# Optimization experiments

Measured on AMD Instinct MI355X. Metric: run time of the kernel, lower is better.

Reference implementation:

```python
import jax, jax.numpy as jnp
import numpy as np

H = 256       # hidden_size
W2V = 300     # word embedding dim
POS = 30      # pos embedding dim
NF = 100      # filters per n-gram CNN
VOCAB = 50000
NPOS = 100
N_EDUS = 1024
L = 20        # tokens per EDU


def setup_inputs() -> dict:
    key = jax.random.key(0)
    ks = jax.random.split(key, 22)
    def nrm(k, shape, s=0.05):
        return jax.random.normal(k, shape, dtype=jnp.float32) * s
    cw = W2V + POS  # CNN input width = 330
    # valid transition sequence: S, then (S, R) repeated n-1 times -> 2n-1 steps
    transes = jnp.concatenate([jnp.zeros((1,), jnp.int32),
                               jnp.tile(jnp.array([0, 1], jnp.int32), N_EDUS - 1)])
    return {
        "edu_words": jax.random.randint(ks[0], (N_EDUS, L), 0, VOCAB),
        "edu_poses": jax.random.randint(ks[1], (N_EDUS, L), 0, NPOS),
        "transes": transes,
        "word_emb": nrm(ks[2], (VOCAB, W2V), 1.0),
        "pos_emb": nrm(ks[3], (NPOS, POS), 1.0),
        "Wu": nrm(ks[4], (NF, 1, 1, cw)), "bu": nrm(ks[5], (NF,)),
        "Wb": nrm(ks[6], (NF, 1, 2, cw)), "bb": nrm(ks[7], (NF,)),
        "Wt": nrm(ks[8], (NF, 1, 3, cw)), "bt": nrm(ks[9], (NF,)),
        "Wp": nrm(ks[10], (2 * H, 2 * W2V + POS + 3 * NF)), "bp": nrm(ks[11], (2 * H,)),
        "Wih": nrm(ks[12], (4 * H, 3 * H)), "Whh": nrm(ks[13], (4 * H, H)),
        "bih": nrm(ks[14], (4 * H,)), "bhh": nrm(ks[15], (4 * H,)),
        "Wc": nrm(ks[16], (5 * H, 3 * H)), "bc": nrm(ks[17], (5 * H,)),
        "Ws": nrm(ks[18], (2, H)), "bs": nrm(ks[19], (2,)),
    }


def _encode_edus(edu_words, edu_poses, word_emb, pos_emb, Wu, bu, Wb, bb, Wt, bt, Wp, bp):
    we = word_emb[edu_words]                # [N, L, 300]
    pe = pos_emb[edu_poses]                 # [N, L, 30]
    x = jnp.concatenate([we, pe], axis=-1)[:, None, :, :]  # NCHW [N,1,L,330]
    def conv_pool(W, b, pad):
        # kernel spans full width -> output width 1; pad only along time
        y = jax.lax.conv_general_dilated(x, W, (1, 1), ((pad, pad), (0, 0)),
                                         dimension_numbers=("NCHW", "OIHW", "NCHW"))[..., 0]
        return jax.nn.relu(y + b[None, :, None]).max(axis=-1)  # [N, F]
    feats = jnp.concatenate([we[:, 0], we[:, -1], pe[:, 0],
                             conv_pool(Wu, bu, 0), conv_pool(Wb, bb, 1),
                             conv_pool(Wt, bt, 2)], axis=-1)   # [N, 930]
    h, c = jnp.split(feats @ Wp.T + bp, 2, axis=-1)
    return h, c


def _parse_loss(edu_words, edu_poses, transes, word_emb, pos_emb, Wu, bu, Wb, bb, Wt, bt,
                Wp, bp, Wih, Whh, bih, bhh, Wc, bc, Ws, bs):
    eh, ec = _encode_edus(edu_words, edu_poses, word_emb, pos_emb, Wu, bu, Wb, bb, Wt, bt, Wp, bp)
    M = N_EDUS + 2
    buf_h = jnp.concatenate([eh, jnp.zeros((2, H), jnp.float32)], axis=0)
    buf_c = jnp.concatenate([ec, jnp.zeros((2, H), jnp.float32)], axis=0)
    stack_h = jnp.zeros((M, H), jnp.float32)  # slots 0,1 are the initial placeholders
    stack_c = jnp.zeros((M, H), jnp.float32)

    def lstm(xv, h, c):  # torch LSTMCell gate order i,f,g,o
        g = xv @ Wih.T + bih + h @ Whh.T + bhh
        i, f, gg, o = jnp.split(g, 4)
        c2 = jax.nn.sigmoid(f) * c + jax.nn.sigmoid(i) * jnp.tanh(gg)
        return jax.nn.sigmoid(o) * jnp.tanh(c2), c2

    def track(sh, sptr, bptr, th, tc):
        xv = jnp.concatenate([sh[sptr - 1], sh[sptr - 2], buf_h[bptr]])
        return lstm(xv, th, tc)

    sptr = jnp.int32(2)
    bptr = jnp.int32(0)
    th, tc = track(stack_h, sptr, bptr, jnp.zeros(H, jnp.float32), jnp.zeros(H, jnp.float32))

    def step(carry, trans):
        sh, sc, sptr, bptr, th, tc = carry
        logits = th @ Ws.T + bs  # scorer MLP with mlp_layers=1 -> single Linear
        is_shift = trans == 0
        # SHIFT candidate: push buffer front
        sh_s = sh.at[sptr].set(buf_h[bptr])
        sc_s = sc.at[sptr].set(buf_c[bptr])
        # REDUCE candidate: tree-LSTM composition of top two stack items
        h1, c1 = sh[sptr - 1], sc[sptr - 1]
        h2, c2 = sh[sptr - 2], sc[sptr - 2]
        g = jnp.concatenate([h1, h2, th]) @ Wc.T + bc
        a, i, f1, f2, o = jnp.split(g, 5)
        rc = jnp.tanh(a) * jax.nn.sigmoid(i) + jax.nn.sigmoid(f1) * c1 + jax.nn.sigmoid(f2) * c2
        rh = jax.nn.sigmoid(o) * jnp.tanh(rc)
        sh_r = sh.at[sptr - 2].set(rh)
        sc_r = sc.at[sptr - 2].set(rc)
        sh2 = jnp.where(is_shift, sh_s, sh_r)
        sc2 = jnp.where(is_shift, sc_s, sc_r)
        sptr2 = jnp.where(is_shift, sptr + 1, sptr - 1)
        bptr2 = jnp.where(is_shift, bptr + 1, bptr)
        th2, tc2 = track(sh2, sptr2, bptr2, th, tc)
        return (sh2, sc2, sptr2, bptr2, th2, tc2), logits

    _, pred = jax.lax.scan(step, (stack_h, stack_c, sptr, bptr, th, tc), transes)
    logp = jax.nn.log_softmax(pred, axis=-1)
    return -jnp.mean(logp[jnp.arange(transes.shape[0]), transes])


def reference(edu_words, edu_poses, transes, word_emb, pos_emb, Wu, bu, Wb, bb, Wt, bt,
              Wp, bp, Wih, Whh, bih, bhh, Wc, bc, Ws, bs):
    return _parse_loss(edu_words, edu_poses, transes, word_emb, pos_emb, Wu, bu, Wb, bb,
                       Wt, bt, Wp, bp, Wih, Whh, bih, bhh, Wc, bc, Ws, bs)
```

## Files before the change

kernel.cpp:

```cpp
#include <hip/hip_runtime.h>
#include <math.h>

#define NEDU  1024
#define LTOK  20
#define CW    330
#define HDIM  256
#define FEAT  930
#define MSLOT 1026
#define NWG   64

#define O_WCATT 0
#define SZ_WCATT (330*600)
#define O_F     (O_WCATT + SZ_WCATT)
#define SZ_F    (NEDU*FEAT)
#define O_LOSSP 0
#define O_BUFH  (O_F + SZ_F)
#define SZ_BUF  (MSLOT*HDIM)
#define O_BUFC  (O_BUFH + SZ_BUF)
#define O_STKT  (O_BUFC + SZ_BUF)
#define O_THTP  (O_STKT + 2*SZ_BUF)
#define O_RHTP  (O_THTP + 2*1024)
#define O_PART  (O_RHTP + 2*1024)
#define NZERO   (2*SZ_BUF + 4*1024)

#define COMPOSED 0x40000000

typedef unsigned long long u64;

#define AG __HIP_MEMORY_SCOPE_AGENT
__device__ __forceinline__ u64 aload64(const u64* p) {
  return __hip_atomic_load(p, __ATOMIC_RELAXED, AG);
}
__device__ __forceinline__ void astore(unsigned* p, unsigned v) {
  __hip_atomic_store(p, v, __ATOMIC_RELAXED, AG);
}
__device__ __forceinline__ unsigned tagbits(float v, unsigned ver) {
  return (__float_as_uint(v) & ~3u) | (ver & 3u);
}
__device__ __forceinline__ float sigm(float x) { return 1.f / (1.f + expf(-x)); }

__device__ __forceinline__ void sync_lds() {
  asm volatile("s_waitcnt lgkmcnt(0)\n\ts_barrier" ::: "memory");
}

__device__ __forceinline__ void gather1T(const unsigned* base, int lane, unsigned tag,
                                         float* x) {
  const u64* p = (const u64*)base + 2 * lane;
  for (int it = 0;; ++it) {
    const u64 a = aload64(p), b = aload64(p + 1);
    const bool ok = (((unsigned)a & 3u) == tag) & (((unsigned)(a >> 32) & 3u) == tag) &
                    (((unsigned)b & 3u) == tag) & (((unsigned)(b >> 32) & 3u) == tag);
    if (__ballot(ok) == ~0ull) {
      x[0] = __uint_as_float((unsigned)a); x[1] = __uint_as_float((unsigned)(a >> 32));
      x[2] = __uint_as_float((unsigned)b); x[3] = __uint_as_float((unsigned)(b >> 32));
      return;
    }
    if (it > 48) __builtin_amdgcn_s_sleep(1);
  }
}
__device__ __forceinline__ void spin4(const u64* p, u64 a, u64 b, unsigned tag, float* x) {
  for (int it = 0;; ++it) {
    const bool ok = (((unsigned)a & 3u) == tag) & (((unsigned)(a >> 32) & 3u) == tag) &
                    (((unsigned)b & 3u) == tag) & (((unsigned)(b >> 32) & 3u) == tag);
    if (__ballot(ok) == ~0ull) break;
    if (it > 40) __builtin_amdgcn_s_sleep(1);
    a = aload64(p); b = aload64(p + 1);
  }
  x[0] = __uint_as_float((unsigned)a); x[1] = __uint_as_float((unsigned)(a >> 32));
  x[2] = __uint_as_float((unsigned)b); x[3] = __uint_as_float((unsigned)(b >> 32));
}

__global__ void prep_kernel(const float* __restrict__ Wu, const float* __restrict__ Wb,
                            const float* __restrict__ Wt, float* __restrict__ ws) {
  const int i0 = blockIdx.x * blockDim.x + threadIdx.x;
  const int st = gridDim.x * blockDim.x;
  for (int i = i0; i < SZ_WCATT; i += st) {
    const int k = i / 600, c = i - 600 * k;
    float v;
    if (c < 100)      v = Wu[c * 330 + k];
    else if (c < 300) { const int q = c - 100; v = Wb[(q % 100) * 660 + (q / 100) * 330 + k]; }
    else              { const int q = c - 300; v = Wt[(q % 100) * 990 + (q / 100) * 330 + k]; }
    ws[O_WCATT + i] = v;
  }
  unsigned* z = (unsigned*)ws + O_STKT;
  for (int i = i0; i < NZERO; i += st) z[i] = 0u;
  for (int i = i0; i < 2 * HDIM; i += st) {
    ws[O_BUFH + NEDU * HDIM + i] = 0.f;
    ws[O_BUFC + NEDU * HDIM + i] = 0.f;
  }
}

__global__ __launch_bounds__(256) void encode_kernel(
    const int* __restrict__ edu_words, const int* __restrict__ edu_poses,
    const float* __restrict__ word_emb, const float* __restrict__ pos_emb,
    const float* __restrict__ bu, const float* __restrict__ bb,
    const float* __restrict__ bt, float* __restrict__ ws) {
  __shared__ __align__(16) float xlT[CW * LTOK];
  __shared__ float zl[300 * 21];
  __shared__ float convout[300];
  const int n = blockIdx.x, tid = threadIdx.x;
  const float* WcatT = ws + O_WCATT;

  for (int i = tid; i < LTOK * CW; i += 256) {
    const int l = i / CW, k = i - l * CW;
    float v;
    if (k < 300) v = word_emb[(size_t)edu_words[n * LTOK + l] * 300 + k];
    else         v = pos_emb[(size_t)edu_poses[n * LTOK + l] * 30 + (k - 300)];
    xlT[k * LTOK + l] = v;
  }
  __syncthreads();

  for (int f = tid; f < 300; f += 256) {
    float acc[LTOK];
#pragma unroll
    for (int l = 0; l < LTOK; ++l) acc[l] = 0.f;
    for (int k = 0; k < CW; ++k) {
      const float w = WcatT[k * 600 + f];
      const float4* xp = (const float4*)(xlT + k * LTOK);
      union { float4 v[5]; float s[20]; } xu;
      xu.v[0] = xp[0]; xu.v[1] = xp[1]; xu.v[2] = xp[2]; xu.v[3] = xp[3]; xu.v[4] = xp[4];
#pragma unroll
      for (int l = 0; l < LTOK; ++l) acc[l] += w * xu.s[l];
    }
#pragma unroll
    for (int l = 0; l < LTOK; ++l) zl[f * 21 + l] = acc[l];
  }
  __syncthreads();
  if (tid < 200) {
    float m;
    if (tid < 100) {
      const int f = tid; const float b = bu[f];
      m = zl[f * 21] + b;
      for (int l = 1; l < 20; ++l) m = fmaxf(m, zl[f * 21 + l] + b);
    } else {
      const int f = tid - 100; const float b = bb[f];
      const float* z0 = zl + (100 + f) * 21;
      const float* z1 = zl + (200 + f) * 21;
      m = z1[0] + b;
      for (int u = 1; u <= 19; ++u) m = fmaxf(m, z0[u - 1] + z1[u] + b);
      m = fmaxf(m, z0[19] + b);
    }
    convout[tid] = fmaxf(m, 0.f);
  }
  __syncthreads();

  for (int f = tid; f < 300; f += 256) {
    float acc[LTOK];
#pragma unroll
    for (int l = 0; l < LTOK; ++l) acc[l] = 0.f;
    for (int k = 0; k < CW; ++k) {
      const float w = WcatT[k * 600 + 300 + f];
      const float4* xp = (const float4*)(xlT + k * LTOK);
      union { float4 v[5]; float s[20]; } xu;
      xu.v[0] = xp[0]; xu.v[1] = xp[1]; xu.v[2] = xp[2]; xu.v[3] = xp[3]; xu.v[4] = xp[4];
#pragma unroll
      for (int l = 0; l < LTOK; ++l) acc[l] += w * xu.s[l];
    }
#pragma unroll
    for (int l = 0; l < LTOK; ++l) zl[f * 21 + l] = acc[l];
  }
  __syncthreads();
  if (tid < 100) {
    const int f = tid; const float b = bt[f];
    const float* z0 = zl + f * 21;
    const float* z1 = zl + (100 + f) * 21;
    const float* z2 = zl + (200 + f) * 21;
    float m = z2[0] + b;
    m = fmaxf(m, z1[0] + z2[1] + b);
    for (int u = 2; u <= 19; ++u) m = fmaxf(m, z0[u - 2] + z1[u - 1] + z2[u] + b);
    m = fmaxf(m, z0[18] + z1[19] + b);
    m = fmaxf(m, z0[19] + b);
    convout[200 + f] = fmaxf(m, 0.f);
  }
  __syncthreads();

  float* Fr = ws + O_F + (size_t)n * FEAT;
  for (int j = tid; j < FEAT; j += 256) {
    float v;
    if (j < 300)      v = xlT[j * LTOK + 0];
    else if (j < 600) v = xlT[(j - 300) * LTOK + 19];
    else if (j < 630) v = xlT[(j - 300) * LTOK + 0];
    else              v = convout[j - 630];
    Fr[j] = v;
  }
}

__global__ __launch_bounds__(256) void proj_kernel(const float* __restrict__ Wp,
                                                   const float* __restrict__ bp,
                                                   float* __restrict__ ws) {
  __shared__ float As[64][17];
  __shared__ float Bs[64][17];
  const float* F = ws + O_F;
  float* bufh = ws + O_BUFH;
  float* bufc = ws + O_BUFC;
  const int tid = threadIdx.x;
  const int m0 = blockIdx.x * 64, n0 = blockIdx.y * 64;
  const int mm0 = (tid & 15) * 4, nn0 = (tid >> 4) * 4;
  float acc[4][4] = {{0.f}};
  for (int k0 = 0; k0 < FEAT; k0 += 16) {
    for (int i = tid; i < 64 * 16; i += 256) {
      const int mm = i >> 4, kk = i & 15;
      const int gk = k0 + kk;
      As[mm][kk] = (gk < FEAT) ? F[(size_t)(m0 + mm) * FEAT + gk] : 0.f;
      Bs[mm][kk] = (gk < FEAT) ? Wp[(size_t)(n0 + mm) * FEAT + gk] : 0.f;
    }
    __syncthreads();
#pragma unroll
    for (int kk = 0; kk < 16; ++kk) {
      float av[4], bv[4];
#pragma unroll
      for (int i = 0; i < 4; ++i) av[i] = As[mm0 + i][kk];
#pragma unroll
      for (int jj = 0; jj < 4; ++jj) bv[jj] = Bs[nn0 + jj][kk];
#pragma unroll
      for (int i = 0; i < 4; ++i)
#pragma unroll
        for (int jj = 0; jj < 4; ++jj) acc[i][jj] += av[i] * bv[jj];
    }
    __syncthreads();
  }
#pragma unroll
  for (int i = 0; i < 4; ++i) {
    const int m = m0 + mm0 + i;
#pragma unroll
    for (int jj = 0; jj < 4; ++jj) {
      const int nn = n0 + nn0 + jj;
      const float v = acc[i][jj] + bp[nn];
      if (nn < 256) bufh[(size_t)m * 256 + nn] = v;
      else          bufc[(size_t)m * 256 + (nn - 256)] = v;
    }
  }
}

__global__ __launch_bounds__(256, 1) void parse_kernel(
    const int* __restrict__ transes, int nT,
    const float* __restrict__ Wih, const float* __restrict__ Whh,
    const float* __restrict__ bih, const float* __restrict__ bhh,
    const float* __restrict__ Wc, const float* __restrict__ bc,
    const float* __restrict__ Wsc, float* __restrict__ ws) {
  const int tid = threadIdx.x;
  const int lane = tid & 63;
  const int wv = tid >> 6;
  const int bx = blockIdx.x;
  const int j0 = bx * 4;

  const float* bufh = ws + O_BUFH;
  const float* bufc = ws + O_BUFC;
  unsigned* stkT = (unsigned*)ws + O_STKT;
  unsigned* thP  = (unsigned*)ws + O_THTP;
  unsigned* rhP  = (unsigned*)ws + O_RHTP;
  float* lossp   = ws + O_LOSSP;

  __shared__ int   trs[2048];
  __shared__ int   ssrc[MSLOT];
  __shared__ int   vcmp[MSLOT];
  __shared__ float sc_lds[MSLOT][4];
  __shared__ float tc_lds[2][4];
  __shared__ float g_lds[20];
  __shared__ float part_lds[8];

  for (int i = tid; i < 2048; i += 256) trs[i] = (i < nT) ? transes[i] : 0;
  for (int i = tid; i < MSLOT; i += 256) { ssrc[i] = 1024; vcmp[i] = 0; }
  for (int i = tid; i < MSLOT * 4; i += 256) ((float*)sc_lds)[i] = 0.f;
  if (tid < 4) { tc_lds[0][tid] = 0.f; tc_lds[1][tid] = 0.f; }
  __syncthreads();

  float wt[4][16]; float bt_[4];
#pragma unroll
  for (int q = 0; q < 4; ++q) {
    const int rg = wv * 256 + j0 + q;
#pragma unroll
    for (int blk = 0; blk < 3; ++blk) {
      const float4 w = *(const float4*)(Wih + (size_t)rg * 768 + blk * 256 + 4 * lane);
      wt[q][4 * blk + 0] = w.x; wt[q][4 * blk + 1] = w.y;
      wt[q][4 * blk + 2] = w.z; wt[q][4 * blk + 3] = w.w;
    }
    const float4 wh = *(const float4*)(Whh + (size_t)rg * 256 + 4 * lane);
    wt[q][12] = wh.x; wt[q][13] = wh.y; wt[q][14] = wh.z; wt[q][15] = wh.w;
    bt_[q] = bih[rg] + bhh[rg];
  }
  float wcm[5][12]; float bc_[5];
#pragma unroll
  for (int q = 0; q < 5; ++q) {
    const int row = 5 * wv + q, gate = row >> 2, jj = row & 3;
    const int rg = gate * 256 + j0 + jj;
#pragma unroll
    for (int blk = 0; blk < 3; ++blk) {
      const float4 w = *(const float4*)(Wc + (size_t)rg * 768 + blk * 256 + 4 * lane);
      wcm[q][4 * blk + 0] = w.x; wcm[q][4 * blk + 1] = w.y;
      wcm[q][4 * blk + 2] = w.z; wcm[q][4 * blk + 3] = w.w;
    }
    bc_[q] = bc[rg];
  }
  float ws0 = 0.f, ws1 = 0.f;
  if (tid < 4) { ws0 = Wsc[j0 + tid]; ws1 = Wsc[256 + j0 + tid]; }

  unsigned V = 0, vrh = 0;
  int sptr = 2, bptr = 0;
  int ccSlot = -1, ccVer = -1;
  float cc0 = 0.f, cc1 = 0.f, cc2 = 0.f, cc3 = 0.f;

  auto red4 = [&](float& a0, float& a1, float& a2, float& a3) {
#pragma unroll
    for (int off = 32; off; off >>= 1) {
      a0 += __shfl_down(a0, off, 64); a1 += __shfl_down(a1, off, 64);
      a2 += __shfl_down(a2, off, 64); a3 += __shfl_down(a3, off, 64);
    }
  };
  auto red5 = [&](float& a0, float& a1, float& a2, float& a3, float& a4) {
#pragma unroll
    for (int off = 32; off; off >>= 1) {
      a0 += __shfl_down(a0, off, 64); a1 += __shfl_down(a1, off, 64);
      a2 += __shfl_down(a2, off, 64); a3 += __shfl_down(a3, off, 64);
      a4 += __shfl_down(a4, off, 64);
    }
  };

  auto resolveH = [&](int slot, float* x) {
    const int e = ssrc[slot];
    if (e < COMPOSED) {
      const float4 f = *(const float4*)(bufh + (size_t)e * HDIM + 4 * lane);
      x[0] = f.x; x[1] = f.y; x[2] = f.z; x[3] = f.w;
    } else {
      const int ver = e & 0xFFFF;
      if (slot == ccSlot && ver == ccVer) { x[0] = cc0; x[1] = cc1; x[2] = cc2; x[3] = cc3; }
      else gather1T(stkT + (size_t)(ver & 1) * SZ_BUF + (size_t)slot * HDIM, lane,
                    (unsigned)(ver & 3), x);
    }
  };

  auto fin_track = [&]() {
    const float gi = g_lds[tid], gf = g_lds[4 + tid], gg = g_lds[8 + tid], go = g_lds[12 + tid];
    const float cn = sigm(gf) * tc_lds[V & 1][tid] + sigm(gi) * tanhf(gg);
    tc_lds[(V + 1) & 1][tid] = cn;
    const float th = sigm(go) * tanhf(cn);
    astore(thP + ((V + 1) & 1) * 1024 + bx * 16 + tid, tagbits(th, V + 1));
    part_lds[tid] = ws0 * th; part_lds[4 + tid] = ws1 * th;
  };
  auto emit_loss = [&]() {
    float* lp = lossp + (size_t)V * 128 + bx * 2;
    lp[0] = part_lds[0] + part_lds[1] + part_lds[2] + part_lds[3];
    lp[1] = part_lds[4] + part_lds[5] + part_lds[6] + part_lds[7];
  };

  {
    const u64* pt = (const u64*)(thP + (V & 1) * 1024) + 8 * lane;
    u64 ta = aload64(pt), tb = aload64(pt + 1);
    float p1[4], p2[4];
    resolveH(1, p1); resolveH(0, p2);
    const float4 f3 = *(const float4*)(bufh + 4 * lane);
    const float p3[4] = { f3.x, f3.y, f3.z, f3.w };
    float s0 = 0.f, s1 = 0.f, s2 = 0.f, s3 = 0.f;
#pragma unroll
    for (int c = 0; c < 4; ++c) {
      s0 += wt[0][c] * p1[c] + wt[0][4 + c] * p2[c] + wt[0][8 + c] * p3[c];
      s1 += wt[1][c] * p1[c] + wt[1][4 + c] * p2[c] + wt[1][8 + c] * p3[c];
      s2 += wt[2][c] * p1[c] + wt[2][4 + c] * p2[c] + wt[2][8 + c] * p3[c];
      s3 += wt[3][c] * p1[c] + wt[3][4 + c] * p2[c] + wt[3][8 + c] * p3[c];
    }
    float xth[4];
    spin4(pt, ta, tb, V & 3, xth);
#pragma unroll
    for (int c = 0; c < 4; ++c) {
      s0 += wt[0][12 + c] * xth[c]; s1 += wt[1][12 + c] * xth[c];
      s2 += wt[2][12 + c] * xth[c]; s3 += wt[3][12 + c] * xth[c];
    }
    red4(s0, s1, s2, s3);
    if (lane == 0) {
      g_lds[wv * 4 + 0] = s0 + bt_[0]; g_lds[wv * 4 + 1] = s1 + bt_[1];
      g_lds[wv * 4 + 2] = s2 + bt_[2]; g_lds[wv * 4 + 3] = s3 + bt_[3];
    }
    sync_lds();
    if (tid < 4) fin_track();
    if (tid == 0) emit_loss();
    sync_lds();
    V = 1;
  }

  for (int t = 0; t < nT; ++t) {
    const int tr = (t < 2048) ? trs[t] : transes[t];
    const u64* pt = (const u64*)(thP + (V & 1) * 1024) + 8 * lane;
    u64 ta = aload64(pt), tb = aload64(pt + 1);
    if (tr) {
      const int sl1 = sptr - 1, sl2 = sptr - 2;
      const int nvS = vcmp[sl2] + 1;
      float h1[4], h2[4];
      resolveH(sl1, h1);
      resolveH(sl2, h2);
      float a0 = 0.f, a1 = 0.f, a2 = 0.f, a3 = 0.f, a4 = 0.f;
#pragma unroll
      for (int c = 0; c < 4; ++c) {
        a0 += wcm[0][c] * h1[c] + wcm[0][4 + c] * h2[c];
        a1 += wcm[1][c] * h1[c] + wcm[1][4 + c] * h2[c];
        a2 += wcm[2][c] * h1[c] + wcm[2][4 + c] * h2[c];
        a3 += wcm[3][c] * h1[c] + wcm[3][4 + c] * h2[c];
        a4 += wcm[4][c] * h1[c] + wcm[4][4 + c] * h2[c];
      }
      float xth[4];
      spin4(pt, ta, tb, V & 3, xth);
#pragma unroll
      for (int c = 0; c < 4; ++c) {
        a0 += wcm[0][8 + c] * xth[c]; a1 += wcm[1][8 + c] * xth[c];
        a2 += wcm[2][8 + c] * xth[c]; a3 += wcm[3][8 + c] * xth[c];
        a4 += wcm[4][8 + c] * xth[c];
      }
      red5(a0, a1, a2, a3, a4);
      if (lane == 0) {
        g_lds[5 * wv + 0] = a0 + bc_[0]; g_lds[5 * wv + 1] = a1 + bc_[1];
        g_lds[5 * wv + 2] = a2 + bc_[2]; g_lds[5 * wv + 3] = a3 + bc_[3];
        g_lds[5 * wv + 4] = a4 + bc_[4];
      }
      sync_lds();
      const unsigned vrh1 = vrh + 1;
      if (tid < 4) {
        const float ga = g_lds[tid], gi = g_lds[4 + tid], gf1 = g_lds[8 + tid],
                    gf2 = g_lds[12 + tid], go = g_lds[16 + tid];
        const float c1 = sc_lds[sl1][tid];
        const float c2 = sc_lds[sl2][tid];
        const float rc = tanhf(ga) * sigm(gi) + sigm(gf1) * c1 + sigm(gf2) * c2;
        const float rh = sigm(go) * tanhf(rc);
        astore(rhP + (vrh1 & 1) * 1024 + bx * 16 + tid, tagbits(rh, vrh1));
        sc_lds[sl2][tid] = rc;
        astore(stkT + (size_t)(nvS & 1) * SZ_BUF + (size_t)sl2 * HDIM + j0 + tid,
               tagbits(rh, (unsigned)nvS));
      }
      if (tid == 0) { vcmp[sl2] = nvS; ssrc[sl2] = COMPOSED | nvS; }
      sync_lds();
      vrh = vrh1;

      const u64* pr = (const u64*)(rhP + (vrh & 1) * 1024) + 8 * lane;
      u64 ra = aload64(pr), rb = aload64(pr + 1);
      float p2[4];
      resolveH(sptr - 3, p2);
      const float4 f3 = *(const float4*)(bufh + (size_t)bptr * HDIM + 4 * lane);
      const float x3[4] = { f3.x, f3.y, f3.z, f3.w };
      float s0 = 0.f, s1 = 0.f, s2 = 0.f, s3 = 0.f;
#pragma unroll
      for (int c = 0; c < 4; ++c) {
        s0 += wt[0][4 + c] * p2[c] + wt[0][8 + c] * x3[c] + wt[0][12 + c] * xth[c];
        s1 += wt[1][4 + c] * p2[c] + wt[1][8 + c] * x3[c] + wt[1][12 + c] * xth[c];
        s2 += wt[2][4 + c] * p2[c] + wt[2][8 + c] * x3[c] + wt[2][12 + c] * xth[c];
        s3 += wt[3][4 + c] * p2[c] + wt[3][8 + c] * x3[c] + wt[3][12 + c] * xth[c];
      }
      float rr[4];
      spin4(pr, ra, rb, vrh & 3, rr);
#pragma unroll
      for (int c = 0; c < 4; ++c) {
        s0 += wt[0][c] * rr[c]; s1 += wt[1][c] * rr[c];
        s2 += wt[2][c] * rr[c]; s3 += wt[3][c] * rr[c];
      }
      red4(s0, s1, s2, s3);
      if (lane == 0) {
        g_lds[wv * 4 + 0] = s0 + bt_[0]; g_lds[wv * 4 + 1] = s1 + bt_[1];
        g_lds[wv * 4 + 2] = s2 + bt_[2]; g_lds[wv * 4 + 3] = s3 + bt_[3];
      }
      sync_lds();
      if (tid < 4) fin_track();
      if (tid == 0) emit_loss();
      sync_lds();
      cc0 = rr[0]; cc1 = rr[1]; cc2 = rr[2]; cc3 = rr[3];
      ccSlot = sl2; ccVer = nvS;
      V += 1; sptr -= 1;
    } else {
      const int slot = sptr;
      if (tid < 4) sc_lds[slot][tid] = bufc[(size_t)bptr * HDIM + j0 + tid];
      if (slot == ccSlot) ccSlot = -1;
      float p2[4];
      resolveH(sptr - 1, p2);
      if (tid == 0) ssrc[slot] = bptr;
      const float4 f1 = *(const float4*)(bufh + (size_t)bptr * HDIM + 4 * lane);
      const float4 f3 = *(const float4*)(bufh + (size_t)(bptr + 1) * HDIM + 4 * lane);
      const float x1[4] = { f1.x, f1.y, f1.z, f1.w };
      const float x3[4] = { f3.x, f3.y, f3.z, f3.w };
      float s0 = 0.f, s1 = 0.f, s2 = 0.f, s3 = 0.f;
#pragma unroll
      for (int c = 0; c < 4; ++c) {
        s0 += wt[0][c] * x1[c] + wt[0][4 + c] * p2[c] + wt[0][8 + c] * x3[c];
        s1 += wt[1][c] * x1[c] + wt[1][4 + c] * p2[c] + wt[1][8 + c] * x3[c];
        s2 += wt[2][c] * x1[c] + wt[2][4 + c] * p2[c] + wt[2][8 + c] * x3[c];
        s3 += wt[3][c] * x1[c] + wt[3][4 + c] * p2[c] + wt[3][8 + c] * x3[c];
      }
      float xth[4];
      spin4(pt, ta, tb, V & 3, xth);
#pragma unroll
      for (int c = 0; c < 4; ++c) {
        s0 += wt[0][12 + c] * xth[c]; s1 += wt[1][12 + c] * xth[c];
        s2 += wt[2][12 + c] * xth[c]; s3 += wt[3][12 + c] * xth[c];
      }
      red4(s0, s1, s2, s3);
      if (lane == 0) {
        g_lds[wv * 4 + 0] = s0 + bt_[0]; g_lds[wv * 4 + 1] = s1 + bt_[1];
        g_lds[wv * 4 + 2] = s2 + bt_[2]; g_lds[wv * 4 + 3] = s3 + bt_[3];
      }
      sync_lds();
      if (tid < 4) fin_track();
      if (tid == 0) emit_loss();
      sync_lds();
      V += 1; sptr += 1; bptr += 1;
    }
  }
}

__global__ __launch_bounds__(256) void loss1_kernel(const int* __restrict__ transes, int nT,
                                                    const float* __restrict__ bsc,
                                                    const float* __restrict__ ws,
                                                    double* __restrict__ part) {
  const int tid = threadIdx.x;
  const int lane = tid & 63, wv = tid >> 6;
  const float* lossp = ws + O_LOSSP;
  __shared__ double red[4];
  const float b0 = bsc[0], b1 = bsc[1];
  double acc = 0.0;
  const int t0 = blockIdx.x * 32 + wv * 8;
  for (int i = 0; i < 8; ++i) {
    const int t = t0 + i;
    if (t < nT) {
      const float2 p = *(const float2*)(lossp + (size_t)t * 128 + 2 * lane);
      float a0 = p.x, a1 = p.y;
#pragma unroll
      for (int off = 32; off; off >>= 1) {
        a0 += __shfl_down(a0, off, 64);
        a1 += __shfl_down(a1, off, 64);
      }
      if (lane == 0) {
        const float l0 = a0 + b0, l1 = a1 + b1;
        const float mx = fmaxf(l0, l1);
        acc += (double)(mx + logf(expf(l0 - mx) + expf(l1 - mx)) - (transes[t] ? l1 : l0));
      }
    }
  }
  if (lane == 0) red[wv] = acc;
  __syncthreads();
  if (tid == 0) part[blockIdx.x] = red[0] + red[1] + red[2] + red[3];
}

__global__ __launch_bounds__(64) void loss2_kernel(int nT, const double* __restrict__ part,
                                                   float* __restrict__ out) {
  double a = part[threadIdx.x];
#pragma unroll
  for (int off = 32; off; off >>= 1) a += __shfl_down(a, off, 64);
  if (threadIdx.x == 0) out[0] = (float)(a / (double)nT);
}

extern "C" void kernel_launch(void* const* d_in, const int* in_sizes, int n_in,
                              void* d_out, int out_size, void* d_ws, size_t ws_size,
                              hipStream_t stream) {
  const int*   edu_words = (const int*)d_in[0];
  const int*   edu_poses = (const int*)d_in[1];
  const int*   transes   = (const int*)d_in[2];
  const float* word_emb  = (const float*)d_in[3];
  const float* pos_emb   = (const float*)d_in[4];
  const float* Wu  = (const float*)d_in[5];
  const float* bu  = (const float*)d_in[6];
  const float* Wb  = (const float*)d_in[7];
  const float* bb  = (const float*)d_in[8];
  const float* Wt  = (const float*)d_in[9];
  const float* bt  = (const float*)d_in[10];
  const float* Wp  = (const float*)d_in[11];
  const float* bp  = (const float*)d_in[12];
  const float* Wih = (const float*)d_in[13];
  const float* Whh = (const float*)d_in[14];
  const float* bih = (const float*)d_in[15];
  const float* bhh = (const float*)d_in[16];
  const float* Wc  = (const float*)d_in[17];
  const float* bc  = (const float*)d_in[18];
  const float* Wsc = (const float*)d_in[19];
  const float* bsc = (const float*)d_in[20];
  float* ws  = (float*)d_ws;
  float* out = (float*)d_out;
  int nT = in_sizes[2];

  hipLaunchKernelGGL(prep_kernel, dim3(256), dim3(256), 0, stream, Wu, Wb, Wt, ws);
  hipLaunchKernelGGL(encode_kernel, dim3(NEDU), dim3(256), 0, stream,
                     edu_words, edu_poses, word_emb, pos_emb, bu, bb, bt, ws);
  hipLaunchKernelGGL(proj_kernel, dim3(16, 8), dim3(256), 0, stream, Wp, bp, ws);

  void* args[] = { (void*)&transes, (void*)&nT, (void*)&Wih, (void*)&Whh, (void*)&bih,
                   (void*)&bhh, (void*)&Wc, (void*)&bc, (void*)&Wsc, (void*)&ws };
  hipLaunchCooperativeKernel((const void*)parse_kernel, dim3(NWG), dim3(256), args, 0, stream);

  double* part = (double*)(ws + O_PART);
  hipLaunchKernelGGL(loss1_kernel, dim3(64), dim3(256), 0, stream, transes, nT, bsc,
                     (const float*)ws, part);
  hipLaunchKernelGGL(loss2_kernel, dim3(1), dim3(64), 0, stream, nT,
                     (const double*)part, out);
}
```

Before: 7.192 ms.

## Co-locate parse workgroups on one XCC and poll XCC-local fast buffers

```diff
diff --git a/kernel.cpp b/kernel.cpp
--- a/kernel.cpp
+++ b/kernel.cpp
@@ -8,6 +8,8 @@
 #define FEAT  930
 #define MSLOT 1026
 #define NWG   64
+#define NVOTE 512
+#define NFAST 10
 
 #define O_WCATT 0
 #define SZ_WCATT (330*600)
@@ -18,14 +20,18 @@
 #define SZ_BUF  (MSLOT*HDIM)
 #define O_BUFC  (O_BUFH + SZ_BUF)
 #define O_STKT  (O_BUFC + SZ_BUF)
-#define O_THTP  (O_STKT + 2*SZ_BUF)
-#define O_RHTP  (O_THTP + 2*1024)
-#define O_PART  (O_RHTP + 2*1024)
-#define NZERO   (2*SZ_BUF + 4*1024)
+#define O_THA   (O_STKT + 2*SZ_BUF)
+#define O_THM   (O_THA + 2048)
+#define O_RHA   (O_THM + 2048)
+#define O_RHM   (O_RHA + 2048)
+#define O_PART  (O_RHM + 2048)
+#define O_SYNC  (O_PART + 128)
+#define NZERO   (2*SZ_BUF + 4*2048)
 
 #define COMPOSED 0x40000000
 
 typedef unsigned long long u64;
+typedef unsigned u32x4 __attribute__((ext_vector_type(4)));
 
 #define AG __HIP_MEMORY_SCOPE_AGENT
 __device__ __forceinline__ u64 aload64(const u64* p) {
@@ -41,6 +47,19 @@
 
 __device__ __forceinline__ void sync_lds() {
   asm volatile("s_waitcnt lgkmcnt(0)\n\ts_barrier" ::: "memory");
+}
+
+__device__ __forceinline__ void ld2_sc0(const unsigned* p, u32x4& a, u32x4& b) {
+  asm volatile("global_load_dwordx4 %0, %2, off sc0\n\t"
+               "global_load_dwordx4 %1, %3, off sc0\n\t"
+               "s_waitcnt vmcnt(0)"
+               : "=&v"(a), "=&v"(b) : "v"(p), "v"(p + 4) : "memory");
+}
+__device__ __forceinline__ void ld2_ag(const unsigned* p, u32x4& a, u32x4& b) {
+  asm volatile("global_load_dwordx4 %0, %2, off sc0 sc1\n\t"
+               "global_load_dwordx4 %1, %3, off sc0 sc1\n\t"
+               "s_waitcnt vmcnt(0)"
+               : "=&v"(a), "=&v"(b) : "v"(p), "v"(p + 4) : "memory");
 }
 
 __device__ __forceinline__ void gather1T(const unsigned* base, int lane, unsigned tag,
@@ -58,17 +77,6 @@
     if (it > 48) __builtin_amdgcn_s_sleep(1);
   }
 }
-__device__ __forceinline__ void spin4(const u64* p, u64 a, u64 b, unsigned tag, float* x) {
-  for (int it = 0;; ++it) {
-    const bool ok = (((unsigned)a & 3u) == tag) & (((unsigned)(a >> 32) & 3u) == tag) &
-                    (((unsigned)b & 3u) == tag) & (((unsigned)(b >> 32) & 3u) == tag);
-    if (__ballot(ok) == ~0ull) break;
-    if (it > 40) __builtin_amdgcn_s_sleep(1);
-    a = aload64(p); b = aload64(p + 1);
-  }
-  x[0] = __uint_as_float((unsigned)a); x[1] = __uint_as_float((unsigned)(a >> 32));
-  x[2] = __uint_as_float((unsigned)b); x[3] = __uint_as_float((unsigned)(b >> 32));
-}
 
 __global__ void prep_kernel(const float* __restrict__ Wu, const float* __restrict__ Wb,
                             const float* __restrict__ Wt, float* __restrict__ ws) {
@@ -88,6 +96,7 @@
     ws[O_BUFH + NEDU * HDIM + i] = 0.f;
     ws[O_BUFC + NEDU * HDIM + i] = 0.f;
   }
+  for (int i = i0; i < 16; i += st) ((unsigned*)ws)[O_SYNC + i] = 0u;
 }
 
 __global__ __launch_bounds__(256) void encode_kernel(
@@ -241,14 +250,33 @@
   const int tid = threadIdx.x;
   const int lane = tid & 63;
   const int wv = tid >> 6;
-  const int bx = blockIdx.x;
+
+  unsigned* syncw = (unsigned*)ws + O_SYNC;
+  __shared__ int role_s;
+  __shared__ int win_s;
+  if (tid == 0) {
+    unsigned xcc;
+    asm volatile("s_getreg_b32 %0, hwreg(HW_REG_XCC_ID)" : "=s"(xcc));
+    xcc &= 7u;
+    const unsigned r = atomicAdd(&syncw[xcc], 1u);
+    if (r == NWG - 1) atomicCAS(&syncw[8], 0u, xcc + 1u);
+    unsigned w;
+    do { w = __hip_atomic_load(&syncw[8], __ATOMIC_RELAXED, AG); } while (w == 0u);
+    role_s = (int)r;
+    win_s  = ((w - 1u) == xcc) ? 1 : 0;
+  }
+  __syncthreads();
+  const int bx = role_s;
+  if (!win_s || bx >= NWG) return;
   const int j0 = bx * 4;
 
   const float* bufh = ws + O_BUFH;
   const float* bufc = ws + O_BUFC;
   unsigned* stkT = (unsigned*)ws + O_STKT;
-  unsigned* thP  = (unsigned*)ws + O_THTP;
-  unsigned* rhP  = (unsigned*)ws + O_RHTP;
+  unsigned* thA  = (unsigned*)ws + O_THA;
+  unsigned* thM  = (unsigned*)ws + O_THM;
+  unsigned* rhA  = (unsigned*)ws + O_RHA;
+  unsigned* rhM  = (unsigned*)ws + O_RHM;
   float* lossp   = ws + O_LOSSP;
 
   __shared__ int   trs[2048];
@@ -297,6 +325,7 @@
 
   unsigned V = 0, vrh = 0;
   int sptr = 2, bptr = 0;
+  int fastok = 1, fstreak = 0;
   int ccSlot = -1, ccVer = -1;
   float cc0 = 0.f, cc1 = 0.f, cc2 = 0.f, cc3 = 0.f;
 
@@ -314,6 +343,37 @@
       a2 += __shfl_down(a2, off, 64); a3 += __shfl_down(a3, off, 64);
       a4 += __shfl_down(a4, off, 64);
     }
+  };
+
+  auto spinP = [&](const unsigned* fb, const unsigned* mb, unsigned Vw, float* x) {
+    const unsigned* fp = fb + 16 * lane;
+    const unsigned* mp = mb + 16 * lane;
+    int it = fastok ? 0 : NFAST;
+    for (;; ++it) {
+      u32x4 a, b;
+      if (it < NFAST) ld2_sc0(fp, a, b);
+      else {
+        ld2_ag(mp, a, b);
+        if (it > NFAST + 48) __builtin_amdgcn_s_sleep(1);
+      }
+      const bool ok = (a.y == Vw) & (a.w == Vw) & (b.y == Vw) & (b.w == Vw);
+      if (__ballot(ok) == ~0ull) {
+        x[0] = __uint_as_float(a.x); x[1] = __uint_as_float(a.z);
+        x[2] = __uint_as_float(b.x); x[3] = __uint_as_float(b.z);
+        break;
+      }
+    }
+    if (it >= NFAST) { if (++fstreak > 12) fastok = 0; }
+    else fstreak = 0;
+  };
+
+  auto publish = [&](unsigned* fastBuf, unsigned* mirBuf, int par, int e, float val,
+                     unsigned ver) {
+    const u64 pair = ((u64)ver << 32) | (u64)__float_as_uint(val);
+    u64* pf = (u64*)(fastBuf + par * 1024 + bx * 16 + 2 * e);
+    u64* pm = (u64*)(mirBuf  + par * 1024 + bx * 16 + 2 * e);
+    __hip_atomic_store(pf, pair, __ATOMIC_RELAXED, __HIP_MEMORY_SCOPE_WORKGROUP);
+    __hip_atomic_store(pm, pair, __ATOMIC_RELAXED, AG);
   };
 
   auto resolveH = [&](int slot, float* x) {
@@ -334,7 +394,7 @@
     const float cn = sigm(gf) * tc_lds[V & 1][tid] + sigm(gi) * tanhf(gg);
     tc_lds[(V + 1) & 1][tid] = cn;
     const float th = sigm(go) * tanhf(cn);
-    astore(thP + ((V + 1) & 1) * 1024 + bx * 16 + tid, tagbits(th, V + 1));
+    publish(thA, thM, (V + 1) & 1, tid, th, V + 1);
     part_lds[tid] = ws0 * th; part_lds[4 + tid] = ws1 * th;
   };
   auto emit_loss = [&]() {
@@ -344,8 +404,6 @@
   };
 
   {
-    const u64* pt = (const u64*)(thP + (V & 1) * 1024) + 8 * lane;
-    u64 ta = aload64(pt), tb = aload64(pt + 1);
     float p1[4], p2[4];
     resolveH(1, p1); resolveH(0, p2);
     const float4 f3 = *(const float4*)(bufh + 4 * lane);
@@ -359,7 +417,7 @@
       s3 += wt[3][c] * p1[c] + wt[3][4 + c] * p2[c] + wt[3][8 + c] * p3[c];
     }
     float xth[4];
-    spin4(pt, ta, tb, V & 3, xth);
+    spinP(thA + (V & 1) * 1024, thM + (V & 1) * 1024, V, xth);
 #pragma unroll
     for (int c = 0; c < 4; ++c) {
       s0 += wt[0][12 + c] * xth[c]; s1 += wt[1][12 + c] * xth[c];
@@ -379,8 +437,6 @@
 
   for (int t = 0; t < nT; ++t) {
     const int tr = (t < 2048) ? trs[t] : transes[t];
-    const u64* pt = (const u64*)(thP + (V & 1) * 1024) + 8 * lane;
-    u64 ta = aload64(pt), tb = aload64(pt + 1);
     if (tr) {
       const int sl1 = sptr - 1, sl2 = sptr - 2;
       const int nvS = vcmp[sl2] + 1;
@@ -397,7 +453,7 @@
         a4 += wcm[4][c] * h1[c] + wcm[4][4 + c] * h2[c];
       }
       float xth[4];
-      spin4(pt, ta, tb, V & 3, xth);
+      spinP(thA + (V & 1) * 1024, thM + (V & 1) * 1024, V, xth);
 #pragma unroll
       for (int c = 0; c < 4; ++c) {
         a0 += wcm[0][8 + c] * xth[c]; a1 += wcm[1][8 + c] * xth[c];
@@ -419,7 +475,7 @@
         const float c2 = sc_lds[sl2][tid];
         const float rc = tanhf(ga) * sigm(gi) + sigm(gf1) * c1 + sigm(gf2) * c2;
         const float rh = sigm(go) * tanhf(rc);
-        astore(rhP + (vrh1 & 1) * 1024 + bx * 16 + tid, tagbits(rh, vrh1));
+        publish(rhA, rhM, vrh1 & 1, tid, rh, vrh1);
         sc_lds[sl2][tid] = rc;
         astore(stkT + (size_t)(nvS & 1) * SZ_BUF + (size_t)sl2 * HDIM + j0 + tid,
                tagbits(rh, (unsigned)nvS));
@@ -428,8 +484,6 @@
       sync_lds();
       vrh = vrh1;
 
-      const u64* pr = (const u64*)(rhP + (vrh & 1) * 1024) + 8 * lane;
-      u64 ra = aload64(pr), rb = aload64(pr + 1);
       float p2[4];
       resolveH(sptr - 3, p2);
       const float4 f3 = *(const float4*)(bufh + (size_t)bptr * HDIM + 4 * lane);
@@ -443,7 +497,7 @@
         s3 += wt[3][4 + c] * p2[c] + wt[3][8 + c] * x3[c] + wt[3][12 + c] * xth[c];
       }
       float rr[4];
-      spin4(pr, ra, rb, vrh & 3, rr);
+      spinP(rhA + (vrh & 1) * 1024, rhM + (vrh & 1) * 1024, vrh, rr);
 #pragma unroll
       for (int c = 0; c < 4; ++c) {
         s0 += wt[0][c] * rr[c]; s1 += wt[1][c] * rr[c];
@@ -481,7 +535,7 @@
         s3 += wt[3][c] * x1[c] + wt[3][4 + c] * p2[c] + wt[3][8 + c] * x3[c];
       }
       float xth[4];
-      spin4(pt, ta, tb, V & 3, xth);
+      spinP(thA + (V & 1) * 1024, thM + (V & 1) * 1024, V, xth);
 #pragma unroll
       for (int c = 0; c < 4; ++c) {
         s0 += wt[0][12 + c] * xth[c]; s1 += wt[1][12 + c] * xth[c];
@@ -575,9 +629,8 @@
                      edu_words, edu_poses, word_emb, pos_emb, bu, bb, bt, ws);
   hipLaunchKernelGGL(proj_kernel, dim3(16, 8), dim3(256), 0, stream, Wp, bp, ws);
 
-  void* args[] = { (void*)&transes, (void*)&nT, (void*)&Wih, (void*)&Whh, (void*)&bih,
-                   (void*)&bhh, (void*)&Wc, (void*)&bc, (void*)&Wsc, (void*)&ws };
-  hipLaunchCooperativeKernel((const void*)parse_kernel, dim3(NWG), dim3(256), args, 0, stream);
+  hipLaunchKernelGGL(parse_kernel, dim3(NVOTE), dim3(256), 0, stream,
+                     transes, nT, Wih, Whh, bih, bhh, Wc, bc, Wsc, ws);
 
   double* part = (double*)(ws + O_PART);
   hipLaunchKernelGGL(loss1_kernel, dim3(64), dim3(256), 0, stream, transes, nT, bsc,
```

Result: slower. 12.60 ms (+75.2%).
